# Optimization experiments

Hardware: AMD Instinct MI355X
Metric: run time of the kernel (lower is better)

## Reference

```python
import jax, jax.numpy as jnp
import numpy as np

B, T, C, H, U = 16, 2048, 512, 4, 250
L, R = 1, 1              # l_order, r_order -> depthwise kernel size 3
K = L + R + 1
SMOOTH, NOISE = 1.0, 0.0  # smooth_factor, noise_threshold


def setup_inputs() -> dict:
    key = jax.random.key(0)
    k0, k1, k2, k3 = jax.random.split(key, 4)
    hidden = jax.random.normal(k0, (B, T, C), dtype=jnp.float32)
    mask = jnp.ones((B, 1, T), dtype=jnp.float32)
    target_label_length = jax.random.randint(k1, (B,), 0, U).astype(jnp.int32)
    # parameters
    conv_w = jax.random.normal(k2, (C, 1, K), dtype=jnp.float32) / np.sqrt(K)   # depthwise Conv1d weight [O, I/g=1, K]
    conv_b = jnp.zeros((C,), dtype=jnp.float32)
    lin_w = jax.random.normal(k3, (1, C), dtype=jnp.float32) / np.sqrt(C)       # cif_output Linear(idim, 1)
    lin_b = jnp.zeros((1,), dtype=jnp.float32)
    sigma = jnp.full((H,), 0.5, dtype=jnp.float32)
    sigma_bias = jnp.zeros((H,), dtype=jnp.float32)
    return {
        "hidden": hidden, "mask": mask, "target_label_length": target_label_length,
        "max_token": U, "conv_w": conv_w, "conv_b": conv_b,
        "lin_w": lin_w, "lin_b": lin_b, "sigma": sigma, "sigma_bias": sigma_bias,
    }


def reference(hidden, mask, target_label_length, max_token, conv_w, conv_b, lin_w, lin_b, sigma, sigma_bias):
    b, t, c = hidden.shape
    h = sigma.shape[0]
    # --- alpha prediction branch ---
    context = jnp.swapaxes(hidden, 1, 2)                       # [B, C, T]
    queries = jnp.pad(context, ((0, 0), (0, 0), (L, R)))       # ConstantPad1d((l, r), 0)
    memory = jax.lax.conv_general_dilated(
        queries, conv_w, window_strides=(1,), padding='VALID',
        feature_group_count=c, dimension_numbers=('NCH', 'OIH', 'NCH'))
    memory = memory + conv_b[None, :, None]
    out = jnp.swapaxes(memory + context, 1, 2)                 # [B, T, C]  (dropout = identity in eval)
    out = jax.nn.relu(out)
    out = out @ lin_w.T + lin_b                                # [B, T, 1]
    alphas = jax.nn.relu(jax.nn.sigmoid(out) * SMOOTH - NOISE)
    mask_bt1 = jnp.swapaxes(mask, -1, -2)                      # [B, T, 1]
    alphas = (alphas * mask_bt1)[..., 0]                       # [B, T]
    mask_bt = mask_bt1[..., 0]                                 # [B, T]
    # --- CIF scaling to target length ---
    target_length = target_label_length.astype(jnp.float32)   # [B]
    token_num = alphas.sum(-1)                                 # [B] (pre-scaling, as in torch)
    alphas = alphas * (target_length / token_num)[:, None]
    alignment = jnp.cumsum(alphas, axis=-1)                    # [B, T]
    # --- Gaussian soft-segment attention ---
    fire_positions = jnp.arange(max_token, dtype=alphas.dtype) + 0.5            # [U]
    dist = fire_positions[None, None, :, None] - alignment[:, None, None, :]    # [B, 1, U, T]
    scores = -(dist * sigma[None, :, None, None]) ** 2 + sigma_bias[None, :, None, None]  # [B, H, U, T]
    scores = jnp.where(mask_bt[:, None, None, :] > 0, scores, -jnp.inf)
    weights = jax.nn.softmax(scores, axis=-1)                  # [B, H, U, T]
    n_hidden = hidden.reshape(b, t, h, c // h).transpose(0, 2, 1, 3)            # [B, H, T, Dh]
    acoustic = jnp.einsum('bhut,bhtd->bhud', weights, n_hidden)                 # [B, H, U, Dh]
    acoustic_embeds = acoustic.transpose(0, 2, 1, 3).reshape(b, max_token, c)   # [B, U, C]
    return acoustic_embeds, token_num, alphas
```

## Files before the change

### kernel.cpp

```cpp
#include <hip/hip_runtime.h>

namespace {
constexpr int kB = 16, kT = 2048, kC = 512, kH = 4, kU = 250, kDH = 128;
constexpr int kDS = 4;
constexpr int kDW = 32;
constexpr int kTT = 256;
constexpr int kNST = kT / kTT;
constexpr int kPitch = 2056;
constexpr int kNB = kDS * kH * kB;
}

typedef __attribute__((ext_vector_type(8))) short short8;
typedef __attribute__((ext_vector_type(4))) float float4v;

__device__ __forceinline__ short f2bf(float x) {
    union { float f; unsigned int u; } v; v.f = x;
    unsigned int r = (v.u + 0x7FFFu + ((v.u >> 16) & 1u)) >> 16;
    return (short)r;
}

__global__ __launch_bounds__(1024) void fused_pif(
    const float* __restrict__ hid, const float* __restrict__ mask,
    const int* __restrict__ target, const float* __restrict__ sigma,
    const float* __restrict__ conv_w, const float* __restrict__ conv_b,
    const float* __restrict__ lin_w, const float* __restrict__ lin_b,
    float* __restrict__ alpha_acc, unsigned int* __restrict__ counter,
    float* __restrict__ out_ac, float* __restrict__ out_tok, float* __restrict__ out_alpha)
{
    __shared__ unsigned short bV[kDW * kPitch];
    __shared__ float al_s[kT];
    __shared__ float wedge[2][16][8][8];
    __shared__ float tedge[kNST][8][8];
    __shared__ float woff[16];
    __shared__ float s_tot;

    const int ds = blockIdx.x, h = blockIdx.y, b = blockIdx.z;
    const int tid = threadIdx.x;
    const int wave = tid >> 6, lane = tid & 63;
    const int dl = tid & 7;
    const int p  = tid >> 3;
    const int pl = lane >> 3;
    const int cbase = h * kDH + ds * kDW;
    const int c0g = cbase + dl * 4;

    float cw0[4], cw1[4], cw2[4], cb4[4], lw4[4];
    {
        float4 w0 = *(const float4*)(conv_w + c0g * 3);
        float4 w1 = *(const float4*)(conv_w + c0g * 3 + 4);
        float4 w2 = *(const float4*)(conv_w + c0g * 3 + 8);
        cw0[0] = w0.x; cw1[0] = w0.y; cw2[0] = w0.z;
        cw0[1] = w0.w; cw1[1] = w1.x; cw2[1] = w1.y;
        cw0[2] = w1.z; cw1[2] = w1.w; cw2[2] = w2.x;
        cw0[3] = w2.y; cw1[3] = w2.z; cw2[3] = w2.w;
        *(float4*)cb4 = *(const float4*)(conv_b + c0g);
        *(float4*)lw4 = *(const float4*)(lin_w + c0g);
    }
    float* acc_g = alpha_acc + (size_t)b * kT;
    const float* hrow = hid + (size_t)b * kT * kC + c0g;

    float4 a0, a1;
    {
        const float* s = hrow + (size_t)(2 * p) * kC;
        a0 = *(const float4*)s;
        a1 = *(const float4*)(s + kC);
    }
    for (int st = 0; st < kNST; st++) {
        #pragma unroll
        for (int e = 0; e < 4; e++) {
            unsigned int lo = (unsigned int)(unsigned short)f2bf(((const float*)&a0)[e]);
            unsigned int hi = (unsigned int)(unsigned short)f2bf(((const float*)&a1)[e]);
            *(unsigned int*)&bV[(dl * 4 + e) * kPitch + st * kTT + 2 * p] = lo | (hi << 16);
        }
        if (pl == 7) {
            *(float4*)&wedge[st & 1][wave][dl][0] = a0;
            *(float4*)&wedge[st & 1][wave][dl][4] = a1;
            if (wave == 15) {
                *(float4*)&tedge[st][dl][0] = a0;
                *(float4*)&tedge[st][dl][4] = a1;
            }
        }
        float4 n0 = a0, n1 = a1;
        if (st + 1 < kNST) {
            const float* s = hrow + (size_t)((st + 1) * kTT + 2 * p) * kC;
            n0 = *(const float4*)s;
            n1 = *(const float4*)(s + kC);
        }
        __syncthreads();

        float pm2[4], pm1[4];
        #pragma unroll
        for (int e = 0; e < 4; e++) {
            pm2[e] = __shfl_up(((const float*)&a0)[e], 8, 64);
            pm1[e] = __shfl_up(((const float*)&a1)[e], 8, 64);
        }
        if (pl == 0) {
            if (wave > 0) {
                *(float4*)pm2 = *(const float4*)&wedge[st & 1][wave - 1][dl][0];
                *(float4*)pm1 = *(const float4*)&wedge[st & 1][wave - 1][dl][4];
            } else if (st > 0) {
                *(float4*)pm2 = *(const float4*)&tedge[st - 1][dl][0];
                *(float4*)pm1 = *(const float4*)&tedge[st - 1][dl][4];
            } else {
                pm2[0] = pm2[1] = pm2[2] = pm2[3] = 0.f;
                pm1[0] = pm1[1] = pm1[2] = pm1[3] = 0.f;
            }
        }
        float s_m1 = 0.f, s_0 = 0.f;
        #pragma unroll
        for (int e = 0; e < 4; e++) {
            float x_m2 = pm2[e], x_m1 = pm1[e];
            float x0 = ((const float*)&a0)[e], x1 = ((const float*)&a1)[e];
            float m_a = fmaf(cw0[e], x_m2, fmaf(cw1[e], x_m1, fmaf(cw2[e], x0, cb4[e])));
            float v_a = m_a + x_m1; v_a = v_a > 0.f ? v_a : 0.f;
            s_m1 = fmaf(v_a, lw4[e], s_m1);
            float m_b = fmaf(cw0[e], x_m1, fmaf(cw1[e], x0, fmaf(cw2[e], x1, cb4[e])));
            float v_b = m_b + x0; v_b = v_b > 0.f ? v_b : 0.f;
            s_0 = fmaf(v_b, lw4[e], s_0);
        }
        #pragma unroll
        for (int off = 1; off <= 4; off <<= 1) {
            s_m1 += __shfl_xor(s_m1, off, 64);
            s_0  += __shfl_xor(s_0, off, 64);
        }
        if (dl == 0) {
            const int t0 = st * kTT + 2 * p;
            if (t0 > 0) atomicAdd(acc_g + (t0 - 1), s_m1);
            atomicAdd(acc_g + t0, s_0);
        }
        a0 = n0; a1 = n1;
    }
    if (tid < 8) {
        float sacc = 0.f;
        #pragma unroll
        for (int e = 0; e < 4; e++) {
            float xm1 = tedge[kNST - 1][dl][e];
            float x0  = tedge[kNST - 1][dl][4 + e];
            float m = fmaf(cw0[e], xm1, fmaf(cw1[e], x0, cb4[e]));
            float v = m + x0; v = v > 0.f ? v : 0.f;
            sacc = fmaf(v, lw4[e], sacc);
        }
        #pragma unroll
        for (int off = 1; off <= 4; off <<= 1) sacc += __shfl_xor(sacc, off, 64);
        if (dl == 0) atomicAdd(acc_g + (kT - 1), sacc);
    }

    __syncthreads();
    if (tid == 0) {
        __hip_atomic_fetch_add(counter, 1u, __ATOMIC_RELEASE, __HIP_MEMORY_SCOPE_AGENT);
        long long guard = 0;
        while (__hip_atomic_load(counter, __ATOMIC_RELAXED, __HIP_MEMORY_SCOPE_AGENT) < (unsigned)kNB) {
            __builtin_amdgcn_s_sleep(4);
            if (++guard > (3LL << 20)) break;
        }
    }
    __syncthreads();

    const int lm = lane & 15, quad = lane >> 4;
    const float sig = sigma[h];
    const float lb = lin_b[0];

    float l0 = __hip_atomic_load(acc_g + 2 * tid,     __ATOMIC_RELAXED, __HIP_MEMORY_SCOPE_AGENT);
    float l1 = __hip_atomic_load(acc_g + 2 * tid + 1, __ATOMIC_RELAXED, __HIP_MEMORY_SCOPE_AGENT);
    float2 mv = ((const float2*)(mask + (size_t)b * kT))[tid];
    float aw0 = (1.f / (1.f + expf(-(l0 + lb)))) * mv.x;
    float aw1 = (1.f / (1.f + expf(-(l1 + lb)))) * mv.y;

    const float p0 = aw0, p1v = aw0 + aw1;
    float sc = p1v;
    #pragma unroll
    for (int off = 1; off <= 32; off <<= 1) {
        float v = __shfl_up(sc, off, 64);
        sc = (lane >= off) ? sc + v : sc;
    }
    if (lane == 63) woff[wave] = sc;
    __syncthreads();
    if (tid == 0) {
        float run = 0.f;
        #pragma unroll
        for (int w = 0; w < 16; w++) { float x = woff[w]; woff[w] = run; run += x; }
        s_tot = run;
    }
    __syncthreads();
    const float tot = s_tot;
    const float scale = (tot != 0.f) ? ((float)target[b] / tot) : 0.f;
    const float basev = woff[wave] + (sc - p1v);
    {
        float c0 = (basev + p0) * scale;
        float c1 = (basev + p1v) * scale;
        float2 alv;
        alv.x = (mv.x > 0.f) ? c0 : 1.0e30f;
        alv.y = (mv.y > 0.f) ? c1 : 1.0e30f;
        ((float2*)al_s)[tid] = alv;
    }
    if (ds == 0 && h == 0) {
        if (tid == 0) out_tok[b] = tot;
        float2 oa; oa.x = aw0 * scale; oa.y = aw1 * scale;
        ((float2*)(out_alpha + (size_t)b * kT))[tid] = oa;
    }
    __syncthreads();

    const int u_base = wave * 16;
    const float du = (float)(u_base + lm) + 0.5f;
    const float dusig = du * sig;
    int pos = 0;
    #pragma unroll
    for (int stp = 1024; stp >= 1; stp >>= 1) {
        int np = pos + stp;
        pos = (al_s[np - 1] < du) ? np : pos;
    }
    float d1 = (pos < kT) ? al_s[pos] - du : 3.0e30f;
    float d0 = (pos > 0) ? du - al_s[pos - 1] : 3.0e30f;
    float dmin = fminf(d0, d1);
    float ms = fminf(dmin, 1.0e4f) * sig;
    const float mu_pos = ms * ms;

    float dmax_l = fminf(dmin, 1.0e4f);
    #pragma unroll
    for (int off = 8; off >= 1; off >>= 1) dmax_l = fmaxf(dmax_l, __shfl_xor(dmax_l, off, 64));
    const float c21 = (sig > 1e-3f) ? 21.0f / (sig * sig) : 9.0e60f;
    const float bound = sqrtf(fmaf(dmax_l, dmax_l, c21));
    const float lo_b = (float)u_base + 0.5f - bound;
    const float hi_b = (float)u_base + 15.5f + bound;
    int p_lo = 0, p_hi = 0;
    #pragma unroll
    for (int stp = 1024; stp >= 1; stp >>= 1) {
        int n1 = p_lo + stp; p_lo = (al_s[n1 - 1] < lo_b) ? n1 : p_lo;
        int n2 = p_hi + stp; p_hi = (al_s[n2 - 1] < hi_b) ? n2 : p_hi;
    }
    const int ks_lo = p_lo >> 5;
    const int ks_end = (p_hi + 31) >> 5;

    float4v acc0 = (float4v)(0.f), acc1 = (float4v)(0.f);
    float lsum = 0.f;

    for (int kg = ks_lo; kg < ks_end; kg++) {
        const int kb = kg * 32;
        float alv[8];
        *(float4*)&alv[0] = *(const float4*)&al_s[kb + quad * 8];
        *(float4*)&alv[4] = *(const float4*)&al_s[kb + quad * 8 + 4];

        short8 afrag;
        #pragma unroll
        for (int j = 0; j < 8; j++) {
            float d = fmaf(-alv[j], sig, dusig);
            float e = __expf(fmaf(-d, d, mu_pos));
            lsum += e;
            afrag[j] = f2bf(e);
        }
        short8 bf0 = *(const short8*)&bV[lm * kPitch + kb + quad * 8];
        short8 bf1 = *(const short8*)&bV[(16 + lm) * kPitch + kb + quad * 8];
        acc0 = __builtin_amdgcn_mfma_f32_16x16x32_bf16(afrag, bf0, acc0, 0, 0, 0);
        acc1 = __builtin_amdgcn_mfma_f32_16x16x32_bf16(afrag, bf1, acc1, 0, 0, 0);
    }

    float lv = lsum;
    lv += __shfl_xor(lv, 16, 64);
    lv += __shfl_xor(lv, 32, 64);
    #pragma unroll
    for (int r = 0; r < 4; r++) {
        const int ur = quad * 4 + r;
        float rl = __shfl(lv, ur, 64);
        float linv = (rl > 1e-30f) ? 1.f / rl : 0.f;
        const int u = u_base + ur;
        if (u < kU) {
            float* dst = out_ac + ((size_t)(b * kU + u)) * kC + h * kDH + ds * kDW + lm;
            dst[0]  = acc0[r] * linv;
            dst[16] = acc1[r] * linv;
        }
    }
}

extern "C" void kernel_launch(void* const* d_in, const int* in_sizes, int n_in,
                              void* d_out, int out_size, void* d_ws, size_t ws_size,
                              hipStream_t stream) {
    const float* hid    = (const float*)d_in[0];
    const float* mask   = (const float*)d_in[1];
    const int*   tgt    = (const int*)d_in[2];
    const float* conv_w = (const float*)d_in[4];
    const float* conv_b = (const float*)d_in[5];
    const float* lin_w  = (const float*)d_in[6];
    const float* lin_b  = (const float*)d_in[7];
    const float* sigma  = (const float*)d_in[8];

    float* alpha_acc = (float*)d_ws;
    unsigned int* counter = (unsigned int*)((char*)d_ws + (size_t)kB * kT * 4);

    float* out_ac    = (float*)d_out;
    float* out_tok   = out_ac + (size_t)kB * kU * kC;
    float* out_alpha = out_tok + kB;

    hipMemsetAsync(d_ws, 0, (size_t)kB * kT * 4 + 64, stream);
    fused_pif<<<dim3(kDS, kH, kB), 1024, 0, stream>>>(
        hid, mask, tgt, sigma, conv_w, conv_b, lin_w, lin_b,
        alpha_acc, counter, out_ac, out_tok, out_alpha);
}
```

Before: 157.0 us.

## Replace atomic alpha accumulation with per-slice partials and wave-local time tiles

Each block now writes per-channel-slice partial logits to its own workspace region with plain relaxed stores, instead of atomically adding into a shared per-batch accumulator. After the grid barrier, each thread sums the 16 slice partials. The load phase is also restructured: each wave owns a contiguous 128-timestep range with all loads issued up front, which removes the per-stage __syncthreads and the LDS edge exchange. The memset shrinks to just the counter, and the spin sleep is shortened. The trade-off is more workspace and 16 loads per thread at the reduction.

```diff
diff --git a/kernel.cpp b/kernel.cpp
--- a/kernel.cpp
+++ b/kernel.cpp
@@ -4,10 +4,9 @@
 constexpr int kB = 16, kT = 2048, kC = 512, kH = 4, kU = 250, kDH = 128;
 constexpr int kDS = 4;
 constexpr int kDW = 32;
-constexpr int kTT = 256;
-constexpr int kNST = kT / kTT;
 constexpr int kPitch = 2056;
 constexpr int kNB = kDS * kH * kB;
+constexpr int kNS = 16;
 }
 
 typedef __attribute__((ext_vector_type(8))) short short8;
@@ -24,24 +23,22 @@
     const int* __restrict__ target, const float* __restrict__ sigma,
     const float* __restrict__ conv_w, const float* __restrict__ conv_b,
     const float* __restrict__ lin_w, const float* __restrict__ lin_b,
-    float* __restrict__ alpha_acc, unsigned int* __restrict__ counter,
+    float* __restrict__ part, unsigned int* __restrict__ counter,
     float* __restrict__ out_ac, float* __restrict__ out_tok, float* __restrict__ out_alpha)
 {
     __shared__ unsigned short bV[kDW * kPitch];
     __shared__ float al_s[kT];
-    __shared__ float wedge[2][16][8][8];
-    __shared__ float tedge[kNST][8][8];
     __shared__ float woff[16];
     __shared__ float s_tot;
 
     const int ds = blockIdx.x, h = blockIdx.y, b = blockIdx.z;
     const int tid = threadIdx.x;
     const int wave = tid >> 6, lane = tid & 63;
-    const int dl = tid & 7;
-    const int p  = tid >> 3;
-    const int pl = lane >> 3;
+    const int dl = lane & 7;
+    const int q  = lane >> 3;
     const int cbase = h * kDH + ds * kDW;
     const int c0g = cbase + dl * 4;
+    const int slice = h * kDS + ds;
 
     float cw0[4], cw1[4], cw2[4], cb4[4], lw4[4];
     {
@@ -55,93 +52,105 @@
         *(float4*)cb4 = *(const float4*)(conv_b + c0g);
         *(float4*)lw4 = *(const float4*)(lin_w + c0g);
     }
-    float* acc_g = alpha_acc + (size_t)b * kT;
+    float* pp = part + ((size_t)slice * kB + b) * kT;
     const float* hrow = hid + (size_t)b * kT * kC + c0g;
-
-    float4 a0, a1;
-    {
-        const float* s = hrow + (size_t)(2 * p) * kC;
-        a0 = *(const float4*)s;
-        a1 = *(const float4*)(s + kC);
-    }
-    for (int st = 0; st < kNST; st++) {
-        #pragma unroll
-        for (int e = 0; e < 4; e++) {
-            unsigned int lo = (unsigned int)(unsigned short)f2bf(((const float*)&a0)[e]);
-            unsigned int hi = (unsigned int)(unsigned short)f2bf(((const float*)&a1)[e]);
-            *(unsigned int*)&bV[(dl * 4 + e) * kPitch + st * kTT + 2 * p] = lo | (hi << 16);
-        }
-        if (pl == 7) {
-            *(float4*)&wedge[st & 1][wave][dl][0] = a0;
-            *(float4*)&wedge[st & 1][wave][dl][4] = a1;
-            if (wave == 15) {
-                *(float4*)&tedge[st][dl][0] = a0;
-                *(float4*)&tedge[st][dl][4] = a1;
-            }
-        }
-        float4 n0 = a0, n1 = a1;
-        if (st + 1 < kNST) {
-            const float* s = hrow + (size_t)((st + 1) * kTT + 2 * p) * kC;
-            n0 = *(const float4*)s;
-            n1 = *(const float4*)(s + kC);
-        }
-        __syncthreads();
-
-        float pm2[4], pm1[4];
-        #pragma unroll
-        for (int e = 0; e < 4; e++) {
-            pm2[e] = __shfl_up(((const float*)&a0)[e], 8, 64);
-            pm1[e] = __shfl_up(((const float*)&a1)[e], 8, 64);
-        }
-        if (pl == 0) {
-            if (wave > 0) {
-                *(float4*)pm2 = *(const float4*)&wedge[st & 1][wave - 1][dl][0];
-                *(float4*)pm1 = *(const float4*)&wedge[st & 1][wave - 1][dl][4];
-            } else if (st > 0) {
-                *(float4*)pm2 = *(const float4*)&tedge[st - 1][dl][0];
-                *(float4*)pm1 = *(const float4*)&tedge[st - 1][dl][4];
-            } else {
-                pm2[0] = pm2[1] = pm2[2] = pm2[3] = 0.f;
-                pm1[0] = pm1[1] = pm1[2] = pm1[3] = 0.f;
-            }
-        }
-        float s_m1 = 0.f, s_0 = 0.f;
-        #pragma unroll
-        for (int e = 0; e < 4; e++) {
-            float x_m2 = pm2[e], x_m1 = pm1[e];
-            float x0 = ((const float*)&a0)[e], x1 = ((const float*)&a1)[e];
-            float m_a = fmaf(cw0[e], x_m2, fmaf(cw1[e], x_m1, fmaf(cw2[e], x0, cb4[e])));
-            float v_a = m_a + x_m1; v_a = v_a > 0.f ? v_a : 0.f;
-            s_m1 = fmaf(v_a, lw4[e], s_m1);
-            float m_b = fmaf(cw0[e], x_m1, fmaf(cw1[e], x0, fmaf(cw2[e], x1, cb4[e])));
-            float v_b = m_b + x0; v_b = v_b > 0.f ? v_b : 0.f;
-            s_0 = fmaf(v_b, lw4[e], s_0);
-        }
-        #pragma unroll
-        for (int off = 1; off <= 4; off <<= 1) {
-            s_m1 += __shfl_xor(s_m1, off, 64);
-            s_0  += __shfl_xor(s_0, off, 64);
-        }
-        if (dl == 0) {
-            const int t0 = st * kTT + 2 * p;
-            if (t0 > 0) atomicAdd(acc_g + (t0 - 1), s_m1);
-            atomicAdd(acc_g + t0, s_0);
-        }
-        a0 = n0; a1 = n1;
-    }
-    if (tid < 8) {
+    const int wbase = wave * 128;
+
+    float4 A0[4], A1[4], B0[4], B1[4];
+    float4 h2, h1;
+    h2.x = h2.y = h2.z = h2.w = 0.f;
+    h1 = h2;
+    if (q == 0 && wave > 0) {
+        const float* s = hrow + (size_t)(wbase - 2) * kC;
+        h2 = *(const float4*)s;
+        h1 = *(const float4*)(s + kC);
+    }
+    #pragma unroll
+    for (int k = 0; k < 4; k++) {
+        const float* s = hrow + (size_t)(wbase + k * 16 + 2 * q) * kC;
+        A0[k] = *(const float4*)s;
+        A1[k] = *(const float4*)(s + kC);
+    }
+    float4 Lp0, Lp1;
+    Lp0 = h2; Lp1 = h1;
+
+    #define PROC(kk, Ax, Ay)  {                                                  \
+        const int t0 = wbase + (kk) * 16 + 2 * q;                                \
+        float pm2[4], pm1[4];                                                    \
+        _Pragma("unroll")                                                        \
+        for (int e = 0; e < 4; e++) {                                            \
+            float c2, c1v;                                                       \
+            if ((kk) == 0) { c2 = ((float*)&h2)[e]; c1v = ((float*)&h1)[e]; }    \
+            else {                                                               \
+                c2  = __shfl(((float*)&Lp0)[e], 56 + dl, 64);                    \
+                c1v = __shfl(((float*)&Lp1)[e], 56 + dl, 64);                    \
+            }                                                                    \
+            float s2 = __shfl_up(((float*)&Ax)[e], 8, 64);                       \
+            float s1 = __shfl_up(((float*)&Ay)[e], 8, 64);                       \
+            pm2[e] = (q == 0) ? c2  : s2;                                        \
+            pm1[e] = (q == 0) ? c1v : s1;                                        \
+        }                                                                        \
+        _Pragma("unroll")                                                        \
+        for (int e = 0; e < 4; e++) {                                            \
+            unsigned int lo = (unsigned int)(unsigned short)f2bf(((float*)&Ax)[e]); \
+            unsigned int hi = (unsigned int)(unsigned short)f2bf(((float*)&Ay)[e]); \
+            *(unsigned int*)&bV[(dl * 4 + e) * kPitch + t0] = lo | (hi << 16);   \
+        }                                                                        \
+        float s_m1 = 0.f, s_0 = 0.f;                                             \
+        _Pragma("unroll")                                                        \
+        for (int e = 0; e < 4; e++) {                                            \
+            float x_m2 = pm2[e], x_m1 = pm1[e];                                  \
+            float x0 = ((float*)&Ax)[e], x1 = ((float*)&Ay)[e];                  \
+            float m_a = fmaf(cw0[e], x_m2, fmaf(cw1[e], x_m1, fmaf(cw2[e], x0, cb4[e]))); \
+            float v_a = m_a + x_m1; v_a = v_a > 0.f ? v_a : 0.f;                 \
+            s_m1 = fmaf(v_a, lw4[e], s_m1);                                      \
+            float m_b = fmaf(cw0[e], x_m1, fmaf(cw1[e], x0, fmaf(cw2[e], x1, cb4[e]))); \
+            float v_b = m_b + x0; v_b = v_b > 0.f ? v_b : 0.f;                   \
+            s_0 = fmaf(v_b, lw4[e], s_0);                                        \
+        }                                                                        \
+        _Pragma("unroll")                                                        \
+        for (int off = 1; off <= 4; off <<= 1) {                                 \
+            s_m1 += __shfl_xor(s_m1, off, 64);                                   \
+            s_0  += __shfl_xor(s_0, off, 64);                                    \
+        }                                                                        \
+        if (dl == 0) {                                                           \
+            if (t0 > 0) __hip_atomic_store(pp + (t0 - 1), s_m1,                  \
+                            __ATOMIC_RELAXED, __HIP_MEMORY_SCOPE_AGENT);         \
+            __hip_atomic_store(pp + t0, s_0,                                     \
+                            __ATOMIC_RELAXED, __HIP_MEMORY_SCOPE_AGENT);         \
+        }                                                                        \
+        Lp0 = Ax; Lp1 = Ay; }
+
+    PROC(0, A0[0], A1[0])
+    #pragma unroll
+    for (int k = 0; k < 4; k++) {
+        const float* s = hrow + (size_t)(wbase + 64 + k * 16 + 2 * q) * kC;
+        B0[k] = *(const float4*)s;
+        B1[k] = *(const float4*)(s + kC);
+    }
+    PROC(1, A0[1], A1[1])
+    PROC(2, A0[2], A1[2])
+    PROC(3, A0[3], A1[3])
+    PROC(4, B0[0], B1[0])
+    PROC(5, B0[1], B1[1])
+    PROC(6, B0[2], B1[2])
+    PROC(7, B0[3], B1[3])
+    #undef PROC
+
+    if (wave == 15 && q == 7) {
         float sacc = 0.f;
         #pragma unroll
         for (int e = 0; e < 4; e++) {
-            float xm1 = tedge[kNST - 1][dl][e];
-            float x0  = tedge[kNST - 1][dl][4 + e];
+            float xm1 = ((float*)&Lp0)[e];
+            float x0  = ((float*)&Lp1)[e];
             float m = fmaf(cw0[e], xm1, fmaf(cw1[e], x0, cb4[e]));
             float v = m + x0; v = v > 0.f ? v : 0.f;
             sacc = fmaf(v, lw4[e], sacc);
         }
         #pragma unroll
         for (int off = 1; off <= 4; off <<= 1) sacc += __shfl_xor(sacc, off, 64);
-        if (dl == 0) atomicAdd(acc_g + (kT - 1), sacc);
+        if (dl == 0) __hip_atomic_store(pp + (kT - 1), sacc,
+                         __ATOMIC_RELAXED, __HIP_MEMORY_SCOPE_AGENT);
     }
 
     __syncthreads();
@@ -149,7 +158,7 @@
         __hip_atomic_fetch_add(counter, 1u, __ATOMIC_RELEASE, __HIP_MEMORY_SCOPE_AGENT);
         long long guard = 0;
         while (__hip_atomic_load(counter, __ATOMIC_RELAXED, __HIP_MEMORY_SCOPE_AGENT) < (unsigned)kNB) {
-            __builtin_amdgcn_s_sleep(4);
+            __builtin_amdgcn_s_sleep(2);
             if (++guard > (3LL << 20)) break;
         }
     }
@@ -159,8 +168,15 @@
     const float sig = sigma[h];
     const float lb = lin_b[0];
 
-    float l0 = __hip_atomic_load(acc_g + 2 * tid,     __ATOMIC_RELAXED, __HIP_MEMORY_SCOPE_AGENT);
-    float l1 = __hip_atomic_load(acc_g + 2 * tid + 1, __ATOMIC_RELAXED, __HIP_MEMORY_SCOPE_AGENT);
+    float l0 = 0.f, l1 = 0.f;
+    #pragma unroll
+    for (int s = 0; s < kNS; s++) {
+        unsigned long long uv = __hip_atomic_load(
+            (const unsigned long long*)(part + ((size_t)s * kB + b) * kT + 2 * tid),
+            __ATOMIC_RELAXED, __HIP_MEMORY_SCOPE_AGENT);
+        union { unsigned long long u; float2 f; } cv; cv.u = uv;
+        l0 += cv.f.x; l1 += cv.f.y;
+    }
     float2 mv = ((const float2*)(mask + (size_t)b * kT))[tid];
     float aw0 = (1.f / (1.f + expf(-(l0 + lb)))) * mv.x;
     float aw1 = (1.f / (1.f + expf(-(l1 + lb)))) * mv.y;
@@ -282,15 +298,15 @@
     const float* lin_b  = (const float*)d_in[7];
     const float* sigma  = (const float*)d_in[8];
 
-    float* alpha_acc = (float*)d_ws;
-    unsigned int* counter = (unsigned int*)((char*)d_ws + (size_t)kB * kT * 4);
+    unsigned int* counter = (unsigned int*)d_ws;
+    float* part = (float*)((char*)d_ws + 256);
 
     float* out_ac    = (float*)d_out;
     float* out_tok   = out_ac + (size_t)kB * kU * kC;
     float* out_alpha = out_tok + kB;
 
-    hipMemsetAsync(d_ws, 0, (size_t)kB * kT * 4 + 64, stream);
+    hipMemsetAsync(d_ws, 0, 256, stream);
     fused_pif<<<dim3(kDS, kH, kB), 1024, 0, stream>>>(
         hid, mask, tgt, sigma, conv_w, conv_b, lin_w, lin_b,
-        alpha_acc, counter, out_ac, out_tok, out_alpha);
+        part, counter, out_ac, out_tok, out_alpha);
 }
```

Measured after the change: 147.4 us. -6.1%, faster.
